# Kernel tuning notes

Measured on AMD Instinct MI355X. Metric: run time of the kernel, lower is better.

The kernel has to match this reference:

```python
import jax, jax.numpy as jnp
import numpy as np


def _gather_neighbours(h, idx):
    # h: (B, N, H); idx: (B, N, K) int -> (B, N, K, H)
    B, N, H = h.shape
    K = idx.shape[-1]
    flat = idx.reshape(B, N * K)  # (B, N*K)
    rep = jnp.take_along_axis(h, flat[..., None], axis=1)  # (B, N*K, H)
    return rep.reshape(B, N, K, H)


def _masked_agg(h, idx, mask):
    # gather neighbor hidden states then masked sum over neighbors -> (B, N, H)
    rep = _gather_neighbours(h, idx)
    return jnp.einsum('bnkh,bnk->bnh', rep, mask)


def setup_inputs() -> dict:
    key = jax.random.key(0)
    ks = jax.random.split(key, 12)
    B, N, H, K = 8, 2000, 128, 32
    s = 1.0 / np.sqrt(H)
    return {
        'node_hidden': jax.random.normal(ks[0], (B, N, H), jnp.float32),
        'cell': jax.random.normal(ks[1], (B, N, H), jnp.float32),
        'w_in': jax.random.normal(ks[2], (4, H, H), jnp.float32) * s,
        'w_out': jax.random.normal(ks[3], (4, H, H), jnp.float32) * s,
        'u_in': jax.random.normal(ks[4], (4, H, H), jnp.float32) * s,
        'u_out': jax.random.normal(ks[5], (4, H, H), jnp.float32) * s,
        'b': jax.random.normal(ks[6], (4, H), jnp.float32) * 0.1,
        'in_node_mask': jax.random.uniform(ks[7], (B, N, K), jnp.float32),
        'out_node_mask': jax.random.uniform(ks[8], (B, N, K), jnp.float32),
        'in_node_index': jax.random.randint(ks[9], (B, N, K), 0, N, jnp.int32),
        'out_node_index': jax.random.randint(ks[10], (B, N, K), 0, N, jnp.int32),
        'layer_num': 2,
    }


def reference(node_hidden, cell, w_in, w_out, u_in, u_out, b,
              in_node_mask, out_node_mask, in_node_index, out_node_index,
              layer_num):
    h, c = node_hidden, cell
    for _ in range(layer_num):
        in_agg = _masked_agg(h, in_node_index, in_node_mask)    # (B,N,H)
        out_agg = _masked_agg(h, out_node_index, out_node_mask)  # (B,N,H)
        # gate pre-activations, gate order: i, o, f, cell
        pre = (jnp.einsum('bnh,ghd->gbnd', in_agg, w_in)
               + jnp.einsum('bnh,ghd->gbnd', out_agg, w_out)
               + jnp.einsum('bnh,ghd->gbnd', h, u_in)
               + jnp.einsum('bnh,ghd->gbnd', h, u_out)
               + b[:, None, None, :])
        i_g = jax.nn.sigmoid(pre[0])
        o_g = jax.nn.sigmoid(pre[1])
        f_g = jax.nn.sigmoid(pre[2])
        g = jnp.tanh(pre[3])
        c = f_g * c + i_g * g
        h = o_g * jnp.tanh(c)
    return h
```

## Files before the change

### kernel.cpp

```cpp
#include <hip/hip_runtime.h>
#include <math.h>

#define B_ 8
#define N_ 2000
#define H_ 128
#define K_ 32
#define M_ (B_*N_)
#define KTOT 384
#define NC 512
#define NTILES 32
#define NCHUNK 12

typedef __attribute__((ext_vector_type(8))) short s8_t;
typedef __attribute__((ext_vector_type(4))) float f4_t;

__device__ __forceinline__ unsigned short f2bf(float x) {
    union { float f; unsigned u; } v; v.f = x;
    unsigned r = v.u + 0x7fff + ((v.u >> 16) & 1);
    return (unsigned short)(r >> 16);
}
__device__ __forceinline__ float bf2f(unsigned short b) {
    union { unsigned u; float f; } v; v.u = (unsigned)b << 16; return v.f;
}
__device__ __forceinline__ float sigm_(float x) { return 1.f / (1.f + __expf(-x)); }
__device__ __forceinline__ float tanh_(float x) { return 2.f / (1.f + __expf(-2.f * x)) - 1.f; }

__device__ __forceinline__ float pickv(f4_t A, int m) {
    float ab = (m & 1) ? A.y : A.x;
    float cd = (m & 1) ? A.w : A.z;
    return (m & 2) ? cd : ab;
}
__device__ __forceinline__ float pick4(float u0, float u1, float u2, float u3, int m) {
    float ab = (m & 1) ? u1 : u0;
    float cd = (m & 1) ? u3 : u2;
    return (m & 2) ? cd : ab;
}

__device__ __forceinline__ void split_store(short* ph, short* pl, const float* f) {
    unsigned h[8], l[8];
    #pragma unroll
    for (int i = 0; i < 8; ++i) {
        unsigned short hs = f2bf(f[i]);
        h[i] = hs;
        l[i] = f2bf(f[i] - bf2f(hs));
    }
    uint4 H, L;
    H.x = h[0] | (h[1] << 16); H.y = h[2] | (h[3] << 16);
    H.z = h[4] | (h[5] << 16); H.w = h[6] | (h[7] << 16);
    L.x = l[0] | (l[1] << 16); L.y = l[2] | (l[3] << 16);
    L.z = l[4] | (l[5] << 16); L.w = l[6] | (l[7] << 16);
    *(uint4*)ph = H;
    *(uint4*)pl = L;
}

__global__ __launch_bounds__(512)
void prep_kernel(const float* __restrict__ w_in,
                 const float* __restrict__ w_out,
                 const float* __restrict__ u_in,
                 const float* __restrict__ u_out,
                 unsigned short* __restrict__ wp_hi,
                 unsigned short* __restrict__ wp_lo) {
    int blk = blockIdx.x;
    int ntile = blk / NCHUNK, chunk = blk % NCHUNK;
    int t = threadIdx.x;
    int lane = t >> 3, e = t & 7;
    int col = ntile * 16 + (lane & 15);
    int k = chunk * 32 + (lane >> 4) * 8 + e;
    int d = col >> 2, g = col & 3;
    float v;
    if (k < 128) {
        v = w_in[(g * 128 + k) * 128 + d];
    } else if (k < 256) {
        v = w_out[(g * 128 + (k - 128)) * 128 + d];
    } else {
        int kk = k - 256;
        v = u_in[(g * 128 + kk) * 128 + d] + u_out[(g * 128 + kk) * 128 + d];
    }
    unsigned short hs = f2bf(v);
    wp_hi[(size_t)blk * 512 + t] = hs;
    wp_lo[(size_t)blk * 512 + t] = f2bf(v - bf2f(hs));
}

__global__ __launch_bounds__(512, 4)
void fused_layer(const float* __restrict__ h_src,
                 const int* __restrict__ in_idx,
                 const float* __restrict__ in_mask,
                 const int* __restrict__ out_idx,
                 const float* __restrict__ out_mask,
                 const unsigned short* __restrict__ wp_hi,
                 const unsigned short* __restrict__ wp_lo,
                 const float* __restrict__ bias,
                 const float* __restrict__ c_src,
                 float* __restrict__ c_dst,
                 float* __restrict__ h_dst) {
    __shared__ short As_hi[NCHUNK * 32 * 32];
    __shared__ short As_lo[NCHUNK * 32 * 32];

    int tid = threadIdx.x;
    int row0 = blockIdx.x * 32;

    {
        int r = tid >> 4;
        int p = tid & 15;
        int d0 = p * 8;
        int row = row0 + r;
        int b = row / N_;
        const float* hb = h_src + (size_t)b * N_ * H_;
        const int*   pii = in_idx  + (size_t)row * K_;
        const float* pim = in_mask + (size_t)row * K_;
        const int*   poi = out_idx + (size_t)row * K_;
        const float* pom = out_mask + (size_t)row * K_;

        float ai[8] = {0,0,0,0,0,0,0,0};
        float ao[8] = {0,0,0,0,0,0,0,0};
        #pragma unroll 4
        for (int k = 0; k < K_; ++k) {
            int   ii = pii[k];
            float mi = pim[k];
            int   oi = poi[k];
            float mo = pom[k];
            const float* pv = hb + (size_t)ii * H_ + d0;
            const float* pw = hb + (size_t)oi * H_ + d0;
            float4 v0 = *(const float4*)pv;
            float4 v1 = *(const float4*)(pv + 4);
            float4 w0 = *(const float4*)pw;
            float4 w1 = *(const float4*)(pw + 4);
            ai[0] += mi * v0.x; ai[1] += mi * v0.y; ai[2] += mi * v0.z; ai[3] += mi * v0.w;
            ai[4] += mi * v1.x; ai[5] += mi * v1.y; ai[6] += mi * v1.z; ai[7] += mi * v1.w;
            ao[0] += mo * w0.x; ao[1] += mo * w0.y; ao[2] += mo * w0.z; ao[3] += mo * w0.w;
            ao[4] += mo * w1.x; ao[5] += mo * w1.y; ao[6] += mo * w1.z; ao[7] += mo * w1.w;
        }
        const float* ph = h_src + (size_t)row * H_ + d0;
        float4 u0 = *(const float4*)ph;
        float4 u1 = *(const float4*)(ph + 4);
        float hh[8] = {u0.x, u0.y, u0.z, u0.w, u1.x, u1.y, u1.z, u1.w};

        int ci  = p >> 2;
        int off = (p & 3) * 8;
        int base_in = ((ci)     * 32 + r) * 32 + off;
        int base_ou = ((4 + ci) * 32 + r) * 32 + off;
        int base_hh = ((8 + ci) * 32 + r) * 32 + off;
        split_store(&As_hi[base_in], &As_lo[base_in], ai);
        split_store(&As_hi[base_ou], &As_lo[base_ou], ao);
        split_store(&As_hi[base_hh], &As_lo[base_hh], hh);
    }
    __syncthreads();

    int lane = tid & 63;
    int w = tid >> 6;
    int ml = lane & 15;
    int kg = lane >> 4;

    f4_t zero = {0.f, 0.f, 0.f, 0.f};
    f4_t acc[2][4];
    #pragma unroll
    for (int i = 0; i < 2; ++i)
        #pragma unroll
        for (int j = 0; j < 4; ++j) acc[i][j] = zero;

    int w4 = w * 4;
    #pragma unroll 2
    for (int c = 0; c < NCHUNK; ++c) {
        s8_t a_hi[2], a_lo[2];
        #pragma unroll
        for (int i = 0; i < 2; ++i) {
            int m = i * 16 + ml;
            a_hi[i] = *(const s8_t*)&As_hi[(c * 32 + m) * 32 + kg * 8];
            a_lo[i] = *(const s8_t*)&As_lo[(c * 32 + m) * 32 + kg * 8];
        }
        #pragma unroll
        for (int j = 0; j < 4; ++j) {
            size_t boff = (((size_t)(w4 + j) * NCHUNK + c) * 64 + lane) * 8;
            s8_t b_hi = *(const s8_t*)(wp_hi + boff);
            s8_t b_lo = *(const s8_t*)(wp_lo + boff);
            #pragma unroll
            for (int i = 0; i < 2; ++i) {
                acc[i][j] = __builtin_amdgcn_mfma_f32_16x16x32_bf16(a_hi[i], b_hi, acc[i][j], 0, 0, 0);
                acc[i][j] = __builtin_amdgcn_mfma_f32_16x16x32_bf16(a_hi[i], b_lo, acc[i][j], 0, 0, 0);
                acc[i][j] = __builtin_amdgcn_mfma_f32_16x16x32_bf16(a_lo[i], b_hi, acc[i][j], 0, 0, 0);
            }
        }
    }

    int g    = lane & 3;
    int qrow = lane >> 4;
    int dl   = (lane >> 2) & 3;
    #pragma unroll
    for (int j = 0; j < 4; ++j) {
        int ncol_base = w * 64 + j * 16;
        int d = (ncol_base >> 2) + dl;
        float b0 = bias[0 * 128 + d];
        float b1 = bias[1 * 128 + d];
        float b2 = bias[2 * 128 + d];
        float b3 = bias[3 * 128 + d];
        #pragma unroll
        for (int i = 0; i < 2; ++i) {
            f4_t A = acc[i][j];
            float s0 = pickv(A, g);
            float s1 = pickv(A, g ^ 1);
            float s2 = pickv(A, g ^ 2);
            float s3 = pickv(A, g ^ 3);
            float u0 = s0;
            float u1 = __shfl_xor(s1, 1);
            float u2 = __shfl_xor(s2, 2);
            float u3 = __shfl_xor(s3, 3);
            float p0 = pick4(u0, u1, u2, u3, g) + b0;
            float p1 = pick4(u0, u1, u2, u3, g ^ 1) + b1;
            float p2 = pick4(u0, u1, u2, u3, g ^ 2) + b2;
            float p3 = pick4(u0, u1, u2, u3, g ^ 3) + b3;
            float ig = sigm_(p0);
            float og = sigm_(p1);
            float fg = sigm_(p2);
            float cg = tanh_(p3);
            int row = row0 + i * 16 + qrow * 4 + g;
            size_t off = (size_t)row * H_ + d;
            float c_old = c_src[off];
            float c_new = fg * c_old + ig * cg;
            c_dst[off] = c_new;
            h_dst[off] = og * tanh_(c_new);
        }
    }
}

extern "C" void kernel_launch(void* const* d_in, const int* in_sizes, int n_in,
                              void* d_out, int out_size, void* d_ws, size_t ws_size,
                              hipStream_t stream) {
    const float* node_hidden = (const float*)d_in[0];
    const float* cell        = (const float*)d_in[1];
    const float* w_in        = (const float*)d_in[2];
    const float* w_out       = (const float*)d_in[3];
    const float* u_in        = (const float*)d_in[4];
    const float* u_out       = (const float*)d_in[5];
    const float* bias        = (const float*)d_in[6];
    const float* in_mask     = (const float*)d_in[7];
    const float* out_mask    = (const float*)d_in[8];
    const int*   in_idx      = (const int*)d_in[9];
    const int*   out_idx     = (const int*)d_in[10];
    float* out = (float*)d_out;

    char* p = (char*)d_ws;
    unsigned short* wp_hi = (unsigned short*)p; p += (size_t)NTILES * NCHUNK * 512 * 2;
    unsigned short* wp_lo = (unsigned short*)p; p += (size_t)NTILES * NCHUNK * 512 * 2;
    float* h_buf = (float*)p;                   p += (size_t)M_ * H_ * 4;
    float* c_buf = (float*)p;                   p += (size_t)M_ * H_ * 4;

    prep_kernel<<<NTILES * NCHUNK, 512, 0, stream>>>(w_in, w_out, u_in, u_out, wp_hi, wp_lo);

    fused_layer<<<M_ / 32, 512, 0, stream>>>(
        node_hidden, in_idx, in_mask, out_idx, out_mask,
        wp_hi, wp_lo, bias, cell, c_buf, h_buf);

    fused_layer<<<M_ / 32, 512, 0, stream>>>(
        h_buf, in_idx, in_mask, out_idx, out_mask,
        wp_hi, wp_lo, bias, c_buf, c_buf, out);
}
```

Before: 217.8 us.

## Split fused layer into separate gather-aggregate and tiled gate GEMM kernels

Splits each layer into an aggregation kernel, which gathers neighbour states into pre-split bf16 MFMA-layout buffers in global memory, and a 2D-tiled GEMM+gates kernel that reads those buffers and converts h on the fly. The goal is better parallelism and occupancy for the latency-bound gather, and spreading the GEMM over more blocks. In exchange it adds global round trips for the aggregated operands and extra kernel launches. It also reuses the output buffer as the cell buffer and skips the final cell write.

```diff
diff --git a/kernel.cpp b/kernel.cpp
--- a/kernel.cpp
+++ b/kernel.cpp
@@ -10,6 +10,7 @@
 #define NC 512
 #define NTILES 32
 #define NCHUNK 12
+#define ACHUNK 8
 
 typedef __attribute__((ext_vector_type(8))) short s8_t;
 typedef __attribute__((ext_vector_type(4))) float f4_t;
@@ -34,23 +35,6 @@
     float ab = (m & 1) ? u1 : u0;
     float cd = (m & 1) ? u3 : u2;
     return (m & 2) ? cd : ab;
-}
-
-__device__ __forceinline__ void split_store(short* ph, short* pl, const float* f) {
-    unsigned h[8], l[8];
-    #pragma unroll
-    for (int i = 0; i < 8; ++i) {
-        unsigned short hs = f2bf(f[i]);
-        h[i] = hs;
-        l[i] = f2bf(f[i] - bf2f(hs));
-    }
-    uint4 H, L;
-    H.x = h[0] | (h[1] << 16); H.y = h[2] | (h[3] << 16);
-    H.z = h[4] | (h[5] << 16); H.w = h[6] | (h[7] << 16);
-    L.x = l[0] | (l[1] << 16); L.y = l[2] | (l[3] << 16);
-    L.z = l[4] | (l[5] << 16); L.w = l[6] | (l[7] << 16);
-    *(uint4*)ph = H;
-    *(uint4*)pl = L;
 }
 
 __global__ __launch_bounds__(512)
@@ -81,75 +65,99 @@
     wp_lo[(size_t)blk * 512 + t] = f2bf(v - bf2f(hs));
 }
 
-__global__ __launch_bounds__(512, 4)
-void fused_layer(const float* __restrict__ h_src,
-                 const int* __restrict__ in_idx,
-                 const float* __restrict__ in_mask,
-                 const int* __restrict__ out_idx,
-                 const float* __restrict__ out_mask,
-                 const unsigned short* __restrict__ wp_hi,
-                 const unsigned short* __restrict__ wp_lo,
-                 const float* __restrict__ bias,
-                 const float* __restrict__ c_src,
-                 float* __restrict__ c_dst,
-                 float* __restrict__ h_dst) {
-    __shared__ short As_hi[NCHUNK * 32 * 32];
-    __shared__ short As_lo[NCHUNK * 32 * 32];
-
+__global__ __launch_bounds__(256)
+void agg_kernel(const float* __restrict__ h,
+                const int* __restrict__ in_idx,
+                const float* __restrict__ in_mask,
+                const int* __restrict__ out_idx,
+                const float* __restrict__ out_mask,
+                unsigned short* __restrict__ A_hi,
+                unsigned short* __restrict__ A_lo) {
     int tid = threadIdx.x;
-    int row0 = blockIdx.x * 32;
-
+    int r = tid >> 5;
+    int p = tid & 31;
+    int row = blockIdx.x * 8 + r;
+    int b = row / N_;
+    const float* hb = h + (size_t)b * N_ * H_;
+
+    __shared__ int   s_idx[8][64];
+    __shared__ float s_msk[8][64];
+    for (int e = tid; e < 512; e += 256) {
+        int r2 = e >> 6, q = e & 63;
+        int ridx = blockIdx.x * 8 + r2;
+        if (q < 32) {
+            s_idx[r2][q] = in_idx[ridx * K_ + q];
+            s_msk[r2][q] = in_mask[ridx * K_ + q];
+        } else {
+            s_idx[r2][q] = out_idx[ridx * K_ + (q - 32)];
+            s_msk[r2][q] = out_mask[ridx * K_ + (q - 32)];
+        }
+    }
+    __syncthreads();
+
+    int d0 = p * 4;
+    float ai[4] = {0.f, 0.f, 0.f, 0.f};
+    float ao[4] = {0.f, 0.f, 0.f, 0.f};
+    #pragma unroll 4
+    for (int k = 0; k < K_; ++k) {
+        int   i1 = s_idx[r][k];
+        float m1 = s_msk[r][k];
+        int   i2 = s_idx[r][32 + k];
+        float m2 = s_msk[r][32 + k];
+        float4 v1 = *(const float4*)(hb + (size_t)i1 * H_ + d0);
+        float4 v2 = *(const float4*)(hb + (size_t)i2 * H_ + d0);
+        ai[0] += m1 * v1.x; ai[1] += m1 * v1.y; ai[2] += m1 * v1.z; ai[3] += m1 * v1.w;
+        ao[0] += m2 * v2.x; ao[1] += m2 * v2.y; ao[2] += m2 * v2.z; ao[3] += m2 * v2.w;
+    }
+
+    int mtile = row >> 4;
+    int kg = (p >> 1) & 3;
+    int e0 = (p & 1) * 4;
+    int lane = (row & 15) + 16 * kg;
+    size_t bi = ((size_t)(mtile * ACHUNK + (p >> 3)) * 64 + lane) * 8 + e0;
+    size_t bo = ((size_t)(mtile * ACHUNK + 4 + (p >> 3)) * 64 + lane) * 8 + e0;
+
+    ushort4 hi_i, lo_i, hi_o, lo_o;
     {
-        int r = tid >> 4;
-        int p = tid & 15;
-        int d0 = p * 8;
-        int row = row0 + r;
-        int b = row / N_;
-        const float* hb = h_src + (size_t)b * N_ * H_;
-        const int*   pii = in_idx  + (size_t)row * K_;
-        const float* pim = in_mask + (size_t)row * K_;
-        const int*   poi = out_idx + (size_t)row * K_;
-        const float* pom = out_mask + (size_t)row * K_;
-
-        float ai[8] = {0,0,0,0,0,0,0,0};
-        float ao[8] = {0,0,0,0,0,0,0,0};
-        #pragma unroll 4
-        for (int k = 0; k < K_; ++k) {
-            int   ii = pii[k];
-            float mi = pim[k];
-            int   oi = poi[k];
-            float mo = pom[k];
-            const float* pv = hb + (size_t)ii * H_ + d0;
-            const float* pw = hb + (size_t)oi * H_ + d0;
-            float4 v0 = *(const float4*)pv;
-            float4 v1 = *(const float4*)(pv + 4);
-            float4 w0 = *(const float4*)pw;
-            float4 w1 = *(const float4*)(pw + 4);
-            ai[0] += mi * v0.x; ai[1] += mi * v0.y; ai[2] += mi * v0.z; ai[3] += mi * v0.w;
-            ai[4] += mi * v1.x; ai[5] += mi * v1.y; ai[6] += mi * v1.z; ai[7] += mi * v1.w;
-            ao[0] += mo * w0.x; ao[1] += mo * w0.y; ao[2] += mo * w0.z; ao[3] += mo * w0.w;
-            ao[4] += mo * w1.x; ao[5] += mo * w1.y; ao[6] += mo * w1.z; ao[7] += mo * w1.w;
-        }
-        const float* ph = h_src + (size_t)row * H_ + d0;
-        float4 u0 = *(const float4*)ph;
-        float4 u1 = *(const float4*)(ph + 4);
-        float hh[8] = {u0.x, u0.y, u0.z, u0.w, u1.x, u1.y, u1.z, u1.w};
-
-        int ci  = p >> 2;
-        int off = (p & 3) * 8;
-        int base_in = ((ci)     * 32 + r) * 32 + off;
-        int base_ou = ((4 + ci) * 32 + r) * 32 + off;
-        int base_hh = ((8 + ci) * 32 + r) * 32 + off;
-        split_store(&As_hi[base_in], &As_lo[base_in], ai);
-        split_store(&As_hi[base_ou], &As_lo[base_ou], ao);
-        split_store(&As_hi[base_hh], &As_lo[base_hh], hh);
-    }
-    __syncthreads();
-
+        unsigned short h0 = f2bf(ai[0]), h1 = f2bf(ai[1]), h2 = f2bf(ai[2]), h3 = f2bf(ai[3]);
+        hi_i = make_ushort4(h0, h1, h2, h3);
+        lo_i = make_ushort4(f2bf(ai[0] - bf2f(h0)), f2bf(ai[1] - bf2f(h1)),
+                            f2bf(ai[2] - bf2f(h2)), f2bf(ai[3] - bf2f(h3)));
+        unsigned short g0 = f2bf(ao[0]), g1 = f2bf(ao[1]), g2 = f2bf(ao[2]), g3 = f2bf(ao[3]);
+        hi_o = make_ushort4(g0, g1, g2, g3);
+        lo_o = make_ushort4(f2bf(ao[0] - bf2f(g0)), f2bf(ao[1] - bf2f(g1)),
+                            f2bf(ao[2] - bf2f(g2)), f2bf(ao[3] - bf2f(g3)));
+    }
+    *(ushort4*)(A_hi + bi) = hi_i;
+    *(ushort4*)(A_lo + bi) = lo_i;
+    *(ushort4*)(A_hi + bo) = hi_o;
+    *(ushort4*)(A_lo + bo) = lo_o;
+}
+
+__global__ __launch_bounds__(256, 4)
+void gemm_gates(const unsigned short* __restrict__ A_hi,
+                const unsigned short* __restrict__ A_lo,
+                const float* __restrict__ h_src,
+                const unsigned short* __restrict__ wp_hi,
+                const unsigned short* __restrict__ wp_lo,
+                const float* __restrict__ bias,
+                const float* __restrict__ c_src,
+                float* __restrict__ c_dst,
+                float* __restrict__ h_dst,
+                int write_c) {
+    int tid  = threadIdx.x;
+    int mt   = blockIdx.x;
+    int jt   = blockIdx.y;
     int lane = tid & 63;
-    int w = tid >> 6;
+    int w    = tid >> 6;
+    int row0 = mt * 64;
+    int m_off = (w & 1) * 32;
+    int n_off = (w >> 1) * 64;
     int ml = lane & 15;
     int kg = lane >> 4;
+
+    int mtile0 = mt * 4 + (w & 1) * 2;
+    int ntile0 = jt * 8 + (w >> 1) * 4;
 
     f4_t zero = {0.f, 0.f, 0.f, 0.f};
     f4_t acc[2][4];
@@ -158,28 +166,65 @@
         #pragma unroll
         for (int j = 0; j < 4; ++j) acc[i][j] = zero;
 
-    int w4 = w * 4;
-    #pragma unroll 2
-    for (int c = 0; c < NCHUNK; ++c) {
-        s8_t a_hi[2], a_lo[2];
+    #pragma unroll 1
+    for (int c = 0; c < ACHUNK; ++c) {
+        s8_t a_hi[2], a_lo[2], b_hi[4], b_lo[4];
         #pragma unroll
         for (int i = 0; i < 2; ++i) {
-            int m = i * 16 + ml;
-            a_hi[i] = *(const s8_t*)&As_hi[(c * 32 + m) * 32 + kg * 8];
-            a_lo[i] = *(const s8_t*)&As_lo[(c * 32 + m) * 32 + kg * 8];
+            size_t off = ((size_t)((mtile0 + i) * ACHUNK + c) * 64 + lane) * 8;
+            a_hi[i] = *(const s8_t*)(A_hi + off);
+            a_lo[i] = *(const s8_t*)(A_lo + off);
         }
         #pragma unroll
         for (int j = 0; j < 4; ++j) {
-            size_t boff = (((size_t)(w4 + j) * NCHUNK + c) * 64 + lane) * 8;
-            s8_t b_hi = *(const s8_t*)(wp_hi + boff);
-            s8_t b_lo = *(const s8_t*)(wp_lo + boff);
+            size_t boff = ((size_t)((ntile0 + j) * NCHUNK + c) * 64 + lane) * 8;
+            b_hi[j] = *(const s8_t*)(wp_hi + boff);
+            b_lo[j] = *(const s8_t*)(wp_lo + boff);
+        }
+        #pragma unroll
+        for (int i = 0; i < 2; ++i)
             #pragma unroll
-            for (int i = 0; i < 2; ++i) {
-                acc[i][j] = __builtin_amdgcn_mfma_f32_16x16x32_bf16(a_hi[i], b_hi, acc[i][j], 0, 0, 0);
-                acc[i][j] = __builtin_amdgcn_mfma_f32_16x16x32_bf16(a_hi[i], b_lo, acc[i][j], 0, 0, 0);
-                acc[i][j] = __builtin_amdgcn_mfma_f32_16x16x32_bf16(a_lo[i], b_hi, acc[i][j], 0, 0, 0);
+            for (int j = 0; j < 4; ++j) {
+                acc[i][j] = __builtin_amdgcn_mfma_f32_16x16x32_bf16(a_hi[i], b_hi[j], acc[i][j], 0, 0, 0);
+                acc[i][j] = __builtin_amdgcn_mfma_f32_16x16x32_bf16(a_hi[i], b_lo[j], acc[i][j], 0, 0, 0);
+                acc[i][j] = __builtin_amdgcn_mfma_f32_16x16x32_bf16(a_lo[i], b_hi[j], acc[i][j], 0, 0, 0);
             }
-        }
+    }
+
+    #pragma unroll 1
+    for (int c = ACHUNK; c < NCHUNK; ++c) {
+        s8_t a_hi[2], a_lo[2], b_hi[4], b_lo[4];
+        #pragma unroll
+        for (int i = 0; i < 2; ++i) {
+            const float* ph = h_src + (size_t)(row0 + m_off + i * 16 + ml) * H_
+                              + (c - ACHUNK) * 32 + kg * 8;
+            float4 f0 = *(const float4*)ph;
+            float4 f1 = *(const float4*)(ph + 4);
+            float fv[8] = {f0.x, f0.y, f0.z, f0.w, f1.x, f1.y, f1.z, f1.w};
+            s8_t hv, lv;
+            #pragma unroll
+            for (int e = 0; e < 8; ++e) {
+                unsigned short hs = f2bf(fv[e]);
+                hv[e] = (short)hs;
+                lv[e] = (short)f2bf(fv[e] - bf2f(hs));
+            }
+            a_hi[i] = hv;
+            a_lo[i] = lv;
+        }
+        #pragma unroll
+        for (int j = 0; j < 4; ++j) {
+            size_t boff = ((size_t)((ntile0 + j) * NCHUNK + c) * 64 + lane) * 8;
+            b_hi[j] = *(const s8_t*)(wp_hi + boff);
+            b_lo[j] = *(const s8_t*)(wp_lo + boff);
+        }
+        #pragma unroll
+        for (int i = 0; i < 2; ++i)
+            #pragma unroll
+            for (int j = 0; j < 4; ++j) {
+                acc[i][j] = __builtin_amdgcn_mfma_f32_16x16x32_bf16(a_hi[i], b_hi[j], acc[i][j], 0, 0, 0);
+                acc[i][j] = __builtin_amdgcn_mfma_f32_16x16x32_bf16(a_hi[i], b_lo[j], acc[i][j], 0, 0, 0);
+                acc[i][j] = __builtin_amdgcn_mfma_f32_16x16x32_bf16(a_lo[i], b_hi[j], acc[i][j], 0, 0, 0);
+            }
     }
 
     int g    = lane & 3;
@@ -187,7 +232,7 @@
     int dl   = (lane >> 2) & 3;
     #pragma unroll
     for (int j = 0; j < 4; ++j) {
-        int ncol_base = w * 64 + j * 16;
+        int ncol_base = jt * 128 + n_off + j * 16;
         int d = (ncol_base >> 2) + dl;
         float b0 = bias[0 * 128 + d];
         float b1 = bias[1 * 128 + d];
@@ -212,11 +257,11 @@
             float og = sigm_(p1);
             float fg = sigm_(p2);
             float cg = tanh_(p3);
-            int row = row0 + i * 16 + qrow * 4 + g;
+            int row = row0 + m_off + i * 16 + qrow * 4 + g;
             size_t off = (size_t)row * H_ + d;
             float c_old = c_src[off];
             float c_new = fg * c_old + ig * cg;
-            c_dst[off] = c_new;
+            if (write_c) c_dst[off] = c_new;
             h_dst[off] = og * tanh_(c_new);
         }
     }
@@ -241,16 +286,19 @@
     char* p = (char*)d_ws;
     unsigned short* wp_hi = (unsigned short*)p; p += (size_t)NTILES * NCHUNK * 512 * 2;
     unsigned short* wp_lo = (unsigned short*)p; p += (size_t)NTILES * NCHUNK * 512 * 2;
+    unsigned short* A_hi  = (unsigned short*)p; p += (size_t)(M_/16) * ACHUNK * 512 * 2;
+    unsigned short* A_lo  = (unsigned short*)p; p += (size_t)(M_/16) * ACHUNK * 512 * 2;
     float* h_buf = (float*)p;                   p += (size_t)M_ * H_ * 4;
-    float* c_buf = (float*)p;                   p += (size_t)M_ * H_ * 4;
 
     prep_kernel<<<NTILES * NCHUNK, 512, 0, stream>>>(w_in, w_out, u_in, u_out, wp_hi, wp_lo);
 
-    fused_layer<<<M_ / 32, 512, 0, stream>>>(
-        node_hidden, in_idx, in_mask, out_idx, out_mask,
-        wp_hi, wp_lo, bias, cell, c_buf, h_buf);
-
-    fused_layer<<<M_ / 32, 512, 0, stream>>>(
-        h_buf, in_idx, in_mask, out_idx, out_mask,
-        wp_hi, wp_lo, bias, c_buf, c_buf, out);
-}
+    agg_kernel<<<M_ / 8, 256, 0, stream>>>(node_hidden, in_idx, in_mask,
+                                           out_idx, out_mask, A_hi, A_lo);
+    gemm_gates<<<dim3(M_ / 64, 4), 256, 0, stream>>>(
+        A_hi, A_lo, node_hidden, wp_hi, wp_lo, bias, cell, out, h_buf, 1);
+
+    agg_kernel<<<M_ / 8, 256, 0, stream>>>(h_buf, in_idx, in_mask,
+                                           out_idx, out_mask, A_hi, A_lo);
+    gemm_gates<<<dim3(M_ / 64, 4), 256, 0, stream>>>(
+        A_hi, A_lo, h_buf, wp_hi, wp_lo, bias, out, out, out, 0);
+}
```

Measured after the change: 210.0 us. 3.6% less time.
